# Performance work log

Hardware: AMD Instinct MI355X
Metric: run time of the kernel (lower is better)

The kernel has to match this reference:

```python
import jax, jax.numpy as jnp
import numpy as np

H = 1024
F = 3584
E = 8
TOP_K = 2
B, S = 2, 1024


def setup_inputs() -> dict:
    key = jax.random.key(0)
    ks = jax.random.split(key, 5)
    scale_h = 1.0 / np.sqrt(H)
    scale_f = 1.0 / np.sqrt(F)
    return {
        "hidden_states": jax.random.normal(ks[0], (B, S, H), dtype=jnp.float32),
        "gate_w": jax.random.normal(ks[1], (H, E), dtype=jnp.float32) * scale_h,
        "w1": jax.random.normal(ks[2], (E, H, F), dtype=jnp.float32) * scale_h,
        "w3": jax.random.normal(ks[3], (E, H, F), dtype=jnp.float32) * scale_h,
        "w2": jax.random.normal(ks[4], (E, F, H), dtype=jnp.float32) * scale_f,
        "top_k": TOP_K,
    }


def reference(hidden_states, gate_w, w1, w3, w2, top_k):
    b, s, h = hidden_states.shape
    e = gate_w.shape[1]
    x = hidden_states.reshape(-1, h)  # [N, H]

    # Router: softmax over experts, top-k selection, renormalize (Mixtral).
    logits = x @ gate_w                             # [N, E]
    probs = jax.nn.softmax(logits, axis=-1)
    rw, sel = jax.lax.top_k(probs, top_k)           # [N, K]
    rw = rw / jnp.sum(rw, axis=-1, keepdims=True)

    # Dispatch/combine weights: combine[n, e] = sum_k rw[n,k] * (sel[n,k]==e).
    # This is the mathematical equivalent of moe_permute + weighted moe_unpermute.
    combine = jnp.sum(jax.nn.one_hot(sel, e, dtype=rw.dtype) * rw[..., None], axis=1)  # [N, E]

    # Grouped SwiGLU expert MLPs; loop over the small fixed expert count so the
    # [N, F] intermediate is materialized one expert at a time.
    out = jnp.zeros_like(x)
    for ei in range(e):
        hdn = jax.nn.silu(x @ w1[ei]) * (x @ w3[ei])  # [N, F]
        out = out + combine[:, ei:ei + 1] * (hdn @ w2[ei])
    return out.reshape(b, s, h)
```

## Files before the change

kernel.cpp:

```cpp
#include <hip/hip_runtime.h>
#include <hip/hip_bf16.h>

#define NTOK 2048
#define HD   1024
#define FD   3584
#define NE   8

#define BM 128
#define BN1 64
#define BM2 64
#define BN 128
#define BK 64
#define NIT1 (HD / BK)
#define KS2 2
#define KLEN2 (FD / KS2)
#define NIT2 (KLEN2 / BK)

typedef __attribute__((ext_vector_type(8))) short short8;
typedef __attribute__((ext_vector_type(4))) float f32x4;

__device__ __forceinline__ unsigned short f2bf(float f) {
    __hip_bfloat16 h = __float2bfloat16(f);
    union { __hip_bfloat16 h; unsigned short u; } c; c.h = h;
    return c.u;
}

typedef __attribute__((address_space(1))) const unsigned int g_cu32;
typedef __attribute__((address_space(3))) unsigned int l_u32;
__device__ __forceinline__ void gl16(const void* g, void* l) {
    __builtin_amdgcn_global_load_lds((g_cu32*)g, (l_u32*)(unsigned int)(size_t)l, 16, 0, 0);
}

__global__ void k_router(const float* __restrict__ x, const float* __restrict__ gw,
                         int* __restrict__ sel, float* __restrict__ selw,
                         int* __restrict__ counts) {
    int token = blockIdx.x * 4 + (threadIdx.x >> 6);
    int lane  = threadIdx.x & 63;
    if (token >= NTOK) return;
    const float* xr = x + (size_t)token * HD;
    float acc[NE];
#pragma unroll
    for (int e = 0; e < NE; e++) acc[e] = 0.f;
    for (int h = lane; h < HD; h += 64) {
        float xv = xr[h];
        const float4* g = (const float4*)(gw + (size_t)h * NE);
        float4 g0 = g[0], g1 = g[1];
        acc[0] += xv * g0.x; acc[1] += xv * g0.y; acc[2] += xv * g0.z; acc[3] += xv * g0.w;
        acc[4] += xv * g1.x; acc[5] += xv * g1.y; acc[6] += xv * g1.z; acc[7] += xv * g1.w;
    }
#pragma unroll
    for (int e = 0; e < NE; e++) {
#pragma unroll
        for (int off = 32; off >= 1; off >>= 1) acc[e] += __shfl_xor(acc[e], off, 64);
    }
    if (lane == 0) {
        float m = acc[0];
#pragma unroll
        for (int e = 1; e < NE; e++) m = fmaxf(m, acc[e]);
        float z[NE];
#pragma unroll
        for (int e = 0; e < NE; e++) z[e] = expf(acc[e] - m);
        int e0 = 0; float z0 = z[0];
#pragma unroll
        for (int e = 1; e < NE; e++) if (z[e] > z0) { z0 = z[e]; e0 = e; }
        int e1 = -1; float z1 = -1.f;
#pragma unroll
        for (int e = 0; e < NE; e++) if (e != e0 && z[e] > z1) { z1 = z[e]; e1 = e; }
        float s = z0 + z1;
        sel[token * 2 + 0] = e0; sel[token * 2 + 1] = e1;
        selw[token * 2 + 0] = z0 / s; selw[token * 2 + 1] = z1 / s;
        atomicAdd(&counts[e0], 1);
        atomicAdd(&counts[e1], 1);
    }
}

__global__ void k_scan(const int* __restrict__ counts, int* __restrict__ basep,
                       int* __restrict__ fillc) {
    if (threadIdx.x == 0 && blockIdx.x == 0) {
        int b = 0;
        for (int e = 0; e < NE; e++) { basep[e] = b; b += counts[e]; fillc[e] = 0; }
    }
}

__global__ void k_fill(const int* __restrict__ sel, const float* __restrict__ selw,
                       const int* __restrict__ basep, int* __restrict__ fillc,
                       int* __restrict__ rowmap, int* __restrict__ rowk,
                       float* __restrict__ roww) {
    int n = blockIdx.x * blockDim.x + threadIdx.x;
    if (n >= NTOK) return;
#pragma unroll
    for (int k = 0; k < 2; k++) {
        int e = sel[n * 2 + k];
        int p = atomicAdd(&fillc[e], 1);
        int g = basep[e] + p;
        rowmap[g] = n; rowk[g] = k; roww[g] = selw[n * 2 + k];
    }
}

__global__ void k_cvt(const float* __restrict__ x, unsigned short* __restrict__ xb) {
    size_t i = ((size_t)blockIdx.x * blockDim.x + threadIdx.x) * 8;
    float4 a = *(const float4*)(x + i);
    float4 b = *(const float4*)(x + i + 4);
    unsigned short p[8] __attribute__((aligned(16))) =
        { f2bf(a.x), f2bf(a.y), f2bf(a.z), f2bf(a.w),
          f2bf(b.x), f2bf(b.y), f2bf(b.z), f2bf(b.w) };
    *(uint4*)(xb + i) = *(uint4*)p;
}

__device__ __forceinline__ uint4 pack8(const float4* bv, int c) {
#define BF(r) ((unsigned int)f2bf(((const float*)&bv[r])[c]))
    uint4 u;
    u.x = BF(0) | (BF(1) << 16);
    u.y = BF(2) | (BF(3) << 16);
    u.z = BF(4) | (BF(5) << 16);
    u.w = BF(6) | (BF(7) << 16);
#undef BF
    return u;
}

__global__ __launch_bounds__(256, 2) void k_gemm1(
    const unsigned short* __restrict__ xb,
    const float* __restrict__ w1, const float* __restrict__ w3,
    const int* __restrict__ counts, const int* __restrict__ basep,
    const int* __restrict__ rowmap, unsigned short* __restrict__ act)
{
    const int e = blockIdx.z;
    const int nrows = counts[e];
    const int m0 = blockIdx.y * BM;
    if (m0 >= nrows) return;
    const int f0 = blockIdx.x * BN1;
    const int gbase = basep[e];

    __shared__ __align__(16) unsigned short At[2][BM][BK];
    __shared__ __align__(16) unsigned short B1[2][BN1][BK];
    __shared__ __align__(16) unsigned short B3[2][BN1][BK];

    const int t = threadIdx.x;
    const int lane = t & 63;
    const int w = t >> 6;
    const int wrm = w >> 1, wnn = w & 1;
    const int lr = lane >> 3;
    const int so = ((lane & 7) ^ lr) * 8;

    const unsigned short* asrc[4];
#pragma unroll
    for (int c = 0; c < 4; c++) {
        const int row = (w * 4 + c) * 8 + lr;
        const int tok = rowmap[gbase + min(m0 + row, nrows - 1)];
        asrc[c] = xb + (size_t)tok * HD + so;
    }

    const int nq = t & 15;
    const int kt = (t >> 4) & 7;
    const int half = t >> 7;
    const float* bp = (half ? w3 : w1) + (size_t)e * HD * FD + (size_t)(8 * kt) * FD + f0 + 4 * nq;
    unsigned short* const bb = half ? &B3[0][0][0] : &B1[0][0][0];
    const int BUFS = BN1 * BK;

    f32x4 acc1[4][2], acc3[4][2];
#pragma unroll
    for (int i = 0; i < 4; i++)
#pragma unroll
        for (int j = 0; j < 2; j++) { acc1[i][j] = (f32x4)(0.f); acc3[i][j] = (f32x4)(0.f); }

    const int l15 = lane & 15;
    const int lhi = lane >> 4;
    const int rs = (l15 & 7) * 8;

    float4 bv[8];

#define G1_WRITE(buf_) do {                                                     \
    _Pragma("unroll")                                                           \
    for (int c = 0; c < 4; c++) {                                               \
        const int n = 4 * nq + c;                                               \
        *(uint4*)&bb[(buf_) * BUFS + n * BK + 8 * (kt ^ (n & 7))] = pack8(bv, c); \
    }                                                                           \
} while (0)

#pragma unroll
    for (int r = 0; r < 8; r++) bv[r] = *(const float4*)(bp + (size_t)r * FD);
#pragma unroll
    for (int c = 0; c < 4; c++) gl16(asrc[c], &At[0][(w * 4 + c) * 8][0]);
    G1_WRITE(0);
    if (NIT1 > 1) {
#pragma unroll
        for (int r = 0; r < 8; r++) bv[r] = *(const float4*)(bp + (size_t)(BK + r) * FD);
        asm volatile("s_waitcnt lgkmcnt(0)" ::: "memory");
        asm volatile("s_waitcnt vmcnt(8)" ::: "memory");
    } else {
        asm volatile("s_waitcnt lgkmcnt(0)" ::: "memory");
        asm volatile("s_waitcnt vmcnt(0)" ::: "memory");
    }
    __builtin_amdgcn_s_barrier();

    for (int it = 0; it < NIT1; ++it) {
        const int cur = it & 1;
        const bool more = (it + 1 < NIT1);
        const bool more2 = (it + 2 < NIT1);
        if (more) {
#pragma unroll
            for (int c = 0; c < 4; c++)
                gl16(asrc[c] + (size_t)(it + 1) * BK, &At[cur ^ 1][(w * 4 + c) * 8][0]);
            G1_WRITE(cur ^ 1);
            if (more2) {
                const size_t k0 = (size_t)(it + 2) * BK;
#pragma unroll
                for (int r = 0; r < 8; r++) bv[r] = *(const float4*)(bp + (k0 + r) * FD);
            }
        }
#pragma unroll
        for (int kk = 0; kk < 2; kk++) {
            const int kc = (kk * 32 + lhi * 8) ^ rs;
            short8 af[4], b1f[2], b3f[2];
#pragma unroll
            for (int i = 0; i < 4; i++)
                af[i] = *(const short8*)&At[cur][wrm * 64 + i * 16 + l15][kc];
#pragma unroll
            for (int j = 0; j < 2; j++) {
                b1f[j] = *(const short8*)&B1[cur][wnn * 32 + j * 16 + l15][kc];
                b3f[j] = *(const short8*)&B3[cur][wnn * 32 + j * 16 + l15][kc];
            }
#pragma unroll
            for (int i = 0; i < 4; i++)
#pragma unroll
                for (int j = 0; j < 2; j++) {
                    acc1[i][j] = __builtin_amdgcn_mfma_f32_16x16x32_bf16(af[i], b1f[j], acc1[i][j], 0, 0, 0);
                    acc3[i][j] = __builtin_amdgcn_mfma_f32_16x16x32_bf16(af[i], b3f[j], acc3[i][j], 0, 0, 0);
                }
        }
        if (more) {
            asm volatile("s_waitcnt lgkmcnt(0)" ::: "memory");
            if (more2) asm volatile("s_waitcnt vmcnt(8)" ::: "memory");
            else       asm volatile("s_waitcnt vmcnt(0)" ::: "memory");
        }
        __builtin_amdgcn_s_barrier();
    }

    const int rbase = wrm * 64 + lhi * 4;
    const int cbase = f0 + wnn * 32 + l15;
#pragma unroll
    for (int i = 0; i < 4; i++) {
#pragma unroll
        for (int r = 0; r < 4; r++) {
            const int ml = rbase + i * 16 + r;
            if (m0 + ml < nrows) {
                const size_t rowoff = (size_t)(gbase + m0 + ml) * FD;
#pragma unroll
                for (int j = 0; j < 2; j++) {
                    float y1 = acc1[i][j][r];
                    float y3 = acc3[i][j][r];
                    float sv = (y1 / (1.f + __expf(-y1))) * y3;
                    act[rowoff + cbase + j * 16] = f2bf(sv);
                }
            }
        }
    }
#undef G1_WRITE
}

__global__ __launch_bounds__(256, 3) void k_gemm2(
    const unsigned short* __restrict__ act,
    const float* __restrict__ w2,
    const int* __restrict__ counts, const int* __restrict__ basep,
    const int* __restrict__ rowmap, const int* __restrict__ rowk,
    const float* __restrict__ roww, float* __restrict__ partial)
{
    const int z = blockIdx.z;
    const int e = z >> 1, ks = z & 1;
    const int nrows = counts[e];
    const int m0 = blockIdx.y * BM2;
    if (m0 >= nrows) return;
    const int h0 = blockIdx.x * BN;
    const int gbase = basep[e];
    const int kbase = ks * KLEN2;

    __shared__ __align__(16) unsigned short At[2][BM2][BK];
    __shared__ __align__(16) unsigned short Bt[2][BN][BK];

    const int t = threadIdx.x;
    const int lane = t & 63;
    const int w = t >> 6;
    const int wr2 = w >> 1, wn2 = w & 1;
    const int lr = lane >> 3;
    const int so = ((lane & 7) ^ lr) * 8;

    const unsigned short* asrc[2];
#pragma unroll
    for (int c = 0; c < 2; c++) {
        const int row = (w * 2 + c) * 8 + lr;
        asrc[c] = act + ((size_t)gbase + min(m0 + row, nrows - 1)) * FD + so + kbase;
    }

    const int nq = (lane & 15) | ((w >> 1) << 4);
    const int kt = ((lane >> 4) & 3) | ((w & 1) << 2);
    const float* bp = w2 + (size_t)e * FD * HD + (size_t)(kbase + 8 * kt) * HD + h0 + 4 * nq;
    unsigned short* const bb = &Bt[0][0][0];
    const int BUFS2 = BN * BK;

    f32x4 acc[2][4];
#pragma unroll
    for (int i = 0; i < 2; i++)
#pragma unroll
        for (int j = 0; j < 4; j++) acc[i][j] = (f32x4)(0.f);

    const int l15 = lane & 15;
    const int lhi = lane >> 4;
    const int rs = (l15 & 7) * 8;

    float4 bv[8];

#define G2_WRITE(buf_) do {                                                     \
    _Pragma("unroll")                                                           \
    for (int c = 0; c < 4; c++) {                                               \
        const int n = 4 * nq + c;                                               \
        *(uint4*)&bb[(buf_) * BUFS2 + n * BK + 8 * (kt ^ (n & 7))] = pack8(bv, c); \
    }                                                                           \
} while (0)

#pragma unroll
    for (int r = 0; r < 8; r++) bv[r] = *(const float4*)(bp + (size_t)r * HD);
#pragma unroll
    for (int c = 0; c < 2; c++) gl16(asrc[c], &At[0][(w * 2 + c) * 8][0]);
    G2_WRITE(0);
    if (NIT2 > 1) {
#pragma unroll
        for (int r = 0; r < 8; r++) bv[r] = *(const float4*)(bp + (size_t)(BK + r) * HD);
        asm volatile("s_waitcnt lgkmcnt(0)" ::: "memory");
        asm volatile("s_waitcnt vmcnt(8)" ::: "memory");
    } else {
        asm volatile("s_waitcnt lgkmcnt(0)" ::: "memory");
        asm volatile("s_waitcnt vmcnt(0)" ::: "memory");
    }
    __builtin_amdgcn_s_barrier();

    for (int it = 0; it < NIT2; ++it) {
        const int cur = it & 1;
        const bool more = (it + 1 < NIT2);
        const bool more2 = (it + 2 < NIT2);
        if (more) {
#pragma unroll
            for (int c = 0; c < 2; c++)
                gl16(asrc[c] + (size_t)(it + 1) * BK, &At[cur ^ 1][(w * 2 + c) * 8][0]);
            G2_WRITE(cur ^ 1);
            if (more2) {
                const size_t k0 = (size_t)(it + 2) * BK;
#pragma unroll
                for (int r = 0; r < 8; r++) bv[r] = *(const float4*)(bp + (k0 + r) * HD);
            }
        }
#pragma unroll
        for (int kk = 0; kk < 2; kk++) {
            const int kc = (kk * 32 + lhi * 8) ^ rs;
            short8 af[2], bf[4];
#pragma unroll
            for (int i = 0; i < 2; i++)
                af[i] = *(const short8*)&At[cur][wr2 * 32 + i * 16 + l15][kc];
#pragma unroll
            for (int j = 0; j < 4; j++)
                bf[j] = *(const short8*)&Bt[cur][wn2 * 64 + j * 16 + l15][kc];
#pragma unroll
            for (int i = 0; i < 2; i++)
#pragma unroll
                for (int j = 0; j < 4; j++)
                    acc[i][j] = __builtin_amdgcn_mfma_f32_16x16x32_bf16(af[i], bf[j], acc[i][j], 0, 0, 0);
        }
        if (more) {
            asm volatile("s_waitcnt lgkmcnt(0)" ::: "memory");
            if (more2) asm volatile("s_waitcnt vmcnt(8)" ::: "memory");
            else       asm volatile("s_waitcnt vmcnt(0)" ::: "memory");
        }
        __builtin_amdgcn_s_barrier();
    }

    const int rbase = wr2 * 32 + lhi * 4;
    const int cbase = h0 + wn2 * 64 + l15;
#pragma unroll
    for (int i = 0; i < 2; i++) {
#pragma unroll
        for (int r = 0; r < 4; r++) {
            const int ml = rbase + i * 16 + r;
            if (m0 + ml < nrows) {
                const int grow = gbase + m0 + ml;
                const int tok = rowmap[grow];
                const int slot = rowk[grow];
                const float wv = roww[grow];
                float* op = partial + (((size_t)slot * KS2 + ks) * NTOK + tok) * HD + cbase;
#pragma unroll
                for (int j = 0; j < 4; j++) op[j * 16] = acc[i][j][r] * wv;
            }
        }
    }
#undef G2_WRITE
}

__global__ void k_combine(const float* __restrict__ partial, float* __restrict__ out) {
    size_t i = ((size_t)blockIdx.x * blockDim.x + threadIdx.x) * 4;
    const size_t st = (size_t)NTOK * HD;
    float4 o = *(const float4*)(partial + i);
#pragma unroll
    for (int s = 1; s < 2 * KS2; s++) {
        float4 v = *(const float4*)(partial + (size_t)s * st + i);
        o.x += v.x; o.y += v.y; o.z += v.z; o.w += v.w;
    }
    *(float4*)(out + i) = o;
}

extern "C" void kernel_launch(void* const* d_in, const int* in_sizes, int n_in,
                              void* d_out, int out_size, void* d_ws, size_t ws_size,
                              hipStream_t stream) {
    const float* x  = (const float*)d_in[0];
    const float* gw = (const float*)d_in[1];
    const float* w1 = (const float*)d_in[2];
    const float* w3 = (const float*)d_in[3];
    const float* w2 = (const float*)d_in[4];
    float* out = (float*)d_out;

    char* ws = (char*)d_ws;
    size_t off = 0;
    auto alloc = [&](size_t b) { char* p = ws + off; off += (b + 255) & ~(size_t)255; return p; };
    int*   sel    = (int*)  alloc((size_t)NTOK * 2 * 4);
    float* selw   = (float*)alloc((size_t)NTOK * 2 * 4);
    int*   counts = (int*)  alloc(NE * 4);
    int*   basep  = (int*)  alloc(NE * 4);
    int*   fillc  = (int*)  alloc(NE * 4);
    int*   rowmap = (int*)  alloc((size_t)NTOK * 2 * 4);
    int*   rowk   = (int*)  alloc((size_t)NTOK * 2 * 4);
    float* roww   = (float*)alloc((size_t)NTOK * 2 * 4);
    unsigned short* xb  = (unsigned short*)alloc((size_t)NTOK * HD * 2);
    unsigned short* act = (unsigned short*)alloc((size_t)NTOK * 2 * FD * 2);
    float* partial = (float*)alloc((size_t)2 * KS2 * NTOK * HD * 4);

    hipMemsetAsync(counts, 0, NE * 4, stream);
    k_cvt<<<(NTOK * HD) / (256 * 8), 256, 0, stream>>>(x, xb);
    k_router<<<NTOK / 4, 256, 0, stream>>>(x, gw, sel, selw, counts);
    k_scan<<<1, 64, 0, stream>>>(counts, basep, fillc);
    k_fill<<<NTOK / 256, 256, 0, stream>>>(sel, selw, basep, fillc, rowmap, rowk, roww);
    k_gemm1<<<dim3(FD / BN1, NTOK / BM, NE), 256, 0, stream>>>(xb, w1, w3, counts, basep, rowmap, act);
    k_gemm2<<<dim3(HD / BN, NTOK / BM2, NE * KS2), 256, 0, stream>>>(act, w2, counts, basep, rowmap, rowk, roww, partial);
    k_combine<<<(NTOK * HD) / (256 * 4), 256, 0, stream>>>(partial, out);
}
```

Before: 342.0 us.

## Repack weight tiles as paired-k bf16 words and atomically accumulate expert outputs

Both expert GEMMs now stage the fp32 weight tile into shared memory as 32-bit words, each holding two consecutive k values for one output column. The tile uses a new XOR swizzle, and each thread loads two k-rows of 16 columns, aiming for cheaper conversion, better coalescing and fewer bank conflicts. The second GEMM also drops the partial buffer and the combine kernel, adding its weighted results into a zeroed output with float atomics. This removes a large partial-buffer write and read plus one launch, at the cost of atomic contention and non-deterministic summation order.

Measured after the change: 355.3 us. 3.9% more time.

```diff
diff --git a/kernel.cpp b/kernel.cpp
--- a/kernel.cpp
+++ b/kernel.cpp
@@ -31,6 +31,12 @@
     __builtin_amdgcn_global_load_lds((g_cu32*)g, (l_u32*)(unsigned int)(size_t)l, 16, 0, 0);
 }
 
+__device__ __forceinline__ short8 pfrag(const unsigned int* P, int n, int q) {
+    uint4 v = *(const uint4*)&P[n * 32 + 4 * ((q ^ (n >> 3)) & 7)];
+    union { uint4 u; short8 s; } c; c.u = v;
+    return c.s;
+}
+
 __global__ void k_router(const float* __restrict__ x, const float* __restrict__ gw,
                          int* __restrict__ sel, float* __restrict__ selw,
                          int* __restrict__ counts) {
@@ -105,17 +111,6 @@
         { f2bf(a.x), f2bf(a.y), f2bf(a.z), f2bf(a.w),
           f2bf(b.x), f2bf(b.y), f2bf(b.z), f2bf(b.w) };
     *(uint4*)(xb + i) = *(uint4*)p;
-}
-
-__device__ __forceinline__ uint4 pack8(const float4* bv, int c) {
-#define BF(r) ((unsigned int)f2bf(((const float*)&bv[r])[c]))
-    uint4 u;
-    u.x = BF(0) | (BF(1) << 16);
-    u.y = BF(2) | (BF(3) << 16);
-    u.z = BF(4) | (BF(5) << 16);
-    u.w = BF(6) | (BF(7) << 16);
-#undef BF
-    return u;
 }
 
 __global__ __launch_bounds__(256, 2) void k_gemm1(
@@ -132,8 +127,8 @@
     const int gbase = basep[e];
 
     __shared__ __align__(16) unsigned short At[2][BM][BK];
-    __shared__ __align__(16) unsigned short B1[2][BN1][BK];
-    __shared__ __align__(16) unsigned short B3[2][BN1][BK];
+    __shared__ __align__(16) unsigned int P1[2][BN1 * 32];
+    __shared__ __align__(16) unsigned int P3[2][BN1 * 32];
 
     const int t = threadIdx.x;
     const int lane = t & 63;
@@ -150,12 +145,14 @@
         asrc[c] = xb + (size_t)tok * HD + so;
     }
 
-    const int nq = t & 15;
-    const int kt = (t >> 4) & 7;
+    const int th = t & 127;
+    const int rp = th >> 2;
+    const int c4 = th & 3;
     const int half = t >> 7;
-    const float* bp = (half ? w3 : w1) + (size_t)e * HD * FD + (size_t)(8 * kt) * FD + f0 + 4 * nq;
-    unsigned short* const bb = half ? &B3[0][0][0] : &B1[0][0][0];
-    const int BUFS = BN1 * BK;
+    const float* bp = (half ? w3 : w1) + (size_t)e * HD * FD
+                    + (size_t)(2 * rp) * FD + f0 + c4 * 16;
+    unsigned int* const myP = half ? &P3[0][0] : &P1[0][0];
+    const int PB = BN1 * 32;
 
     f32x4 acc1[4][2], acc3[4][2];
 #pragma unroll
@@ -167,30 +164,36 @@
     const int lhi = lane >> 4;
     const int rs = (l15 & 7) * 8;
 
-    float4 bv[8];
-
-#define G1_WRITE(buf_) do {                                                     \
+    float4 bv0[4], bv1[4];
+
+#define G1_LOADB(koff_) do {                                                    \
     _Pragma("unroll")                                                           \
-    for (int c = 0; c < 4; c++) {                                               \
-        const int n = 4 * nq + c;                                               \
-        *(uint4*)&bb[(buf_) * BUFS + n * BK + 8 * (kt ^ (n & 7))] = pack8(bv, c); \
+    for (int m = 0; m < 4; m++) {                                               \
+        bv0[m] = *(const float4*)(bp + (size_t)(koff_) * FD + 4 * m);           \
+        bv1[m] = *(const float4*)(bp + (size_t)((koff_) + 1) * FD + 4 * m);     \
     }                                                                           \
 } while (0)
 
-#pragma unroll
-    for (int r = 0; r < 8; r++) bv[r] = *(const float4*)(bp + (size_t)r * FD);
+#define G1_WRITEB(buf_) do {                                                    \
+    _Pragma("unroll")                                                           \
+    for (int m = 0; m < 4; m++) {                                               \
+        _Pragma("unroll")                                                       \
+        for (int q = 0; q < 4; q++) {                                           \
+            const int n = c4 * 16 + 4 * m + q;                                  \
+            unsigned int v = (unsigned int)f2bf(((const float*)&bv0[m])[q])     \
+                           | ((unsigned int)f2bf(((const float*)&bv1[m])[q]) << 16); \
+            myP[(buf_) * PB + n * 32 + (rp ^ (((n >> 3) & 7) << 2))] = v;       \
+        }                                                                       \
+    }                                                                           \
+} while (0)
+
+    G1_LOADB(0);
+    G1_WRITEB(0);
 #pragma unroll
     for (int c = 0; c < 4; c++) gl16(asrc[c], &At[0][(w * 4 + c) * 8][0]);
-    G1_WRITE(0);
-    if (NIT1 > 1) {
-#pragma unroll
-        for (int r = 0; r < 8; r++) bv[r] = *(const float4*)(bp + (size_t)(BK + r) * FD);
-        asm volatile("s_waitcnt lgkmcnt(0)" ::: "memory");
-        asm volatile("s_waitcnt vmcnt(8)" ::: "memory");
-    } else {
-        asm volatile("s_waitcnt lgkmcnt(0)" ::: "memory");
-        asm volatile("s_waitcnt vmcnt(0)" ::: "memory");
-    }
+    if (NIT1 > 1) G1_LOADB(BK);
+    asm volatile("s_waitcnt lgkmcnt(0)" ::: "memory");
+    asm volatile("s_waitcnt vmcnt(8)" ::: "memory");
     __builtin_amdgcn_s_barrier();
 
     for (int it = 0; it < NIT1; ++it) {
@@ -201,24 +204,22 @@
 #pragma unroll
             for (int c = 0; c < 4; c++)
                 gl16(asrc[c] + (size_t)(it + 1) * BK, &At[cur ^ 1][(w * 4 + c) * 8][0]);
-            G1_WRITE(cur ^ 1);
-            if (more2) {
-                const size_t k0 = (size_t)(it + 2) * BK;
-#pragma unroll
-                for (int r = 0; r < 8; r++) bv[r] = *(const float4*)(bp + (k0 + r) * FD);
-            }
+            G1_WRITEB(cur ^ 1);
+            if (more2) G1_LOADB((size_t)(it + 2) * BK);
         }
 #pragma unroll
         for (int kk = 0; kk < 2; kk++) {
             const int kc = (kk * 32 + lhi * 8) ^ rs;
+            const int q = kk * 4 + lhi;
             short8 af[4], b1f[2], b3f[2];
 #pragma unroll
             for (int i = 0; i < 4; i++)
                 af[i] = *(const short8*)&At[cur][wrm * 64 + i * 16 + l15][kc];
 #pragma unroll
             for (int j = 0; j < 2; j++) {
-                b1f[j] = *(const short8*)&B1[cur][wnn * 32 + j * 16 + l15][kc];
-                b3f[j] = *(const short8*)&B3[cur][wnn * 32 + j * 16 + l15][kc];
+                const int n = wnn * 32 + j * 16 + l15;
+                b1f[j] = pfrag(&P1[cur][0], n, q);
+                b3f[j] = pfrag(&P3[cur][0], n, q);
             }
 #pragma unroll
             for (int i = 0; i < 4; i++)
@@ -255,7 +256,8 @@
             }
         }
     }
-#undef G1_WRITE
+#undef G1_LOADB
+#undef G1_WRITEB
 }
 
 __global__ __launch_bounds__(256, 3) void k_gemm2(
@@ -263,7 +265,7 @@
     const float* __restrict__ w2,
     const int* __restrict__ counts, const int* __restrict__ basep,
     const int* __restrict__ rowmap, const int* __restrict__ rowk,
-    const float* __restrict__ roww, float* __restrict__ partial)
+    const float* __restrict__ roww, float* __restrict__ out)
 {
     const int z = blockIdx.z;
     const int e = z >> 1, ks = z & 1;
@@ -275,7 +277,7 @@
     const int kbase = ks * KLEN2;
 
     __shared__ __align__(16) unsigned short At[2][BM2][BK];
-    __shared__ __align__(16) unsigned short Bt[2][BN][BK];
+    __shared__ __align__(16) unsigned int P[2][BN * 32];
 
     const int t = threadIdx.x;
     const int lane = t & 63;
@@ -291,11 +293,9 @@
         asrc[c] = act + ((size_t)gbase + min(m0 + row, nrows - 1)) * FD + so + kbase;
     }
 
-    const int nq = (lane & 15) | ((w >> 1) << 4);
-    const int kt = ((lane >> 4) & 3) | ((w & 1) << 2);
-    const float* bp = w2 + (size_t)e * FD * HD + (size_t)(kbase + 8 * kt) * HD + h0 + 4 * nq;
-    unsigned short* const bb = &Bt[0][0][0];
-    const int BUFS2 = BN * BK;
+    const int rp = t >> 3;
+    const int c8 = t & 7;
+    const float* bp = w2 + (size_t)e * FD * HD + (size_t)(kbase + 2 * rp) * HD + h0 + c8 * 16;
 
     f32x4 acc[2][4];
 #pragma unroll
@@ -307,30 +307,36 @@
     const int lhi = lane >> 4;
     const int rs = (l15 & 7) * 8;
 
-    float4 bv[8];
-
-#define G2_WRITE(buf_) do {                                                     \
+    float4 bv0[4], bv1[4];
+
+#define G2_LOADB(koff_) do {                                                    \
     _Pragma("unroll")                                                           \
-    for (int c = 0; c < 4; c++) {                                               \
-        const int n = 4 * nq + c;                                               \
-        *(uint4*)&bb[(buf_) * BUFS2 + n * BK + 8 * (kt ^ (n & 7))] = pack8(bv, c); \
+    for (int m = 0; m < 4; m++) {                                               \
+        bv0[m] = *(const float4*)(bp + (size_t)(koff_) * HD + 4 * m);           \
+        bv1[m] = *(const float4*)(bp + (size_t)((koff_) + 1) * HD + 4 * m);     \
     }                                                                           \
 } while (0)
 
-#pragma unroll
-    for (int r = 0; r < 8; r++) bv[r] = *(const float4*)(bp + (size_t)r * HD);
+#define G2_WRITEB(buf_) do {                                                    \
+    _Pragma("unroll")                                                           \
+    for (int m = 0; m < 4; m++) {                                               \
+        _Pragma("unroll")                                                       \
+        for (int q = 0; q < 4; q++) {                                           \
+            const int n = c8 * 16 + 4 * m + q;                                  \
+            unsigned int v = (unsigned int)f2bf(((const float*)&bv0[m])[q])     \
+                           | ((unsigned int)f2bf(((const float*)&bv1[m])[q]) << 16); \
+            P[buf_][n * 32 + (rp ^ (((n >> 3) & 7) << 2))] = v;                 \
+        }                                                                       \
+    }                                                                           \
+} while (0)
+
+    G2_LOADB(0);
+    G2_WRITEB(0);
 #pragma unroll
     for (int c = 0; c < 2; c++) gl16(asrc[c], &At[0][(w * 2 + c) * 8][0]);
-    G2_WRITE(0);
-    if (NIT2 > 1) {
-#pragma unroll
-        for (int r = 0; r < 8; r++) bv[r] = *(const float4*)(bp + (size_t)(BK + r) * HD);
-        asm volatile("s_waitcnt lgkmcnt(0)" ::: "memory");
-        asm volatile("s_waitcnt vmcnt(8)" ::: "memory");
-    } else {
-        asm volatile("s_waitcnt lgkmcnt(0)" ::: "memory");
-        asm volatile("s_waitcnt vmcnt(0)" ::: "memory");
-    }
+    if (NIT2 > 1) G2_LOADB(BK);
+    asm volatile("s_waitcnt lgkmcnt(0)" ::: "memory");
+    asm volatile("s_waitcnt vmcnt(8)" ::: "memory");
     __builtin_amdgcn_s_barrier();
 
     for (int it = 0; it < NIT2; ++it) {
@@ -341,23 +347,22 @@
 #pragma unroll
             for (int c = 0; c < 2; c++)
                 gl16(asrc[c] + (size_t)(it + 1) * BK, &At[cur ^ 1][(w * 2 + c) * 8][0]);
-            G2_WRITE(cur ^ 1);
-            if (more2) {
-                const size_t k0 = (size_t)(it + 2) * BK;
-#pragma unroll
-                for (int r = 0; r < 8; r++) bv[r] = *(const float4*)(bp + (k0 + r) * HD);
-            }
+            G2_WRITEB(cur ^ 1);
+            if (more2) G2_LOADB((size_t)(it + 2) * BK);
         }
 #pragma unroll
         for (int kk = 0; kk < 2; kk++) {
             const int kc = (kk * 32 + lhi * 8) ^ rs;
+            const int q = kk * 4 + lhi;
             short8 af[2], bf[4];
 #pragma unroll
             for (int i = 0; i < 2; i++)
                 af[i] = *(const short8*)&At[cur][wr2 * 32 + i * 16 + l15][kc];
 #pragma unroll
-            for (int j = 0; j < 4; j++)
-                bf[j] = *(const short8*)&Bt[cur][wn2 * 64 + j * 16 + l15][kc];
+            for (int j = 0; j < 4; j++) {
+                const int n = wn2 * 64 + j * 16 + l15;
+                bf[j] = pfrag(&P[cur][0], n, q);
+            }
 #pragma unroll
             for (int i = 0; i < 2; i++)
 #pragma unroll
@@ -382,27 +387,16 @@
             if (m0 + ml < nrows) {
                 const int grow = gbase + m0 + ml;
                 const int tok = rowmap[grow];
-                const int slot = rowk[grow];
                 const float wv = roww[grow];
-                float* op = partial + (((size_t)slot * KS2 + ks) * NTOK + tok) * HD + cbase;
-#pragma unroll
-                for (int j = 0; j < 4; j++) op[j * 16] = acc[i][j][r] * wv;
+                float* op = out + (size_t)tok * HD + cbase;
+#pragma unroll
+                for (int j = 0; j < 4; j++)
+                    atomicAdd(&op[j * 16], acc[i][j][r] * wv);
             }
         }
     }
-#undef G2_WRITE
-}
-
-__global__ void k_combine(const float* __restrict__ partial, float* __restrict__ out) {
-    size_t i = ((size_t)blockIdx.x * blockDim.x + threadIdx.x) * 4;
-    const size_t st = (size_t)NTOK * HD;
-    float4 o = *(const float4*)(partial + i);
-#pragma unroll
-    for (int s = 1; s < 2 * KS2; s++) {
-        float4 v = *(const float4*)(partial + (size_t)s * st + i);
-        o.x += v.x; o.y += v.y; o.z += v.z; o.w += v.w;
-    }
-    *(float4*)(out + i) = o;
+#undef G2_LOADB
+#undef G2_WRITEB
 }
 
 extern "C" void kernel_launch(void* const* d_in, const int* in_sizes, int n_in,
@@ -428,14 +422,13 @@
     float* roww   = (float*)alloc((size_t)NTOK * 2 * 4);
     unsigned short* xb  = (unsigned short*)alloc((size_t)NTOK * HD * 2);
     unsigned short* act = (unsigned short*)alloc((size_t)NTOK * 2 * FD * 2);
-    float* partial = (float*)alloc((size_t)2 * KS2 * NTOK * HD * 4);
 
     hipMemsetAsync(counts, 0, NE * 4, stream);
+    hipMemsetAsync(out, 0, (size_t)out_size * 4, stream);
     k_cvt<<<(NTOK * HD) / (256 * 8), 256, 0, stream>>>(x, xb);
     k_router<<<NTOK / 4, 256, 0, stream>>>(x, gw, sel, selw, counts);
     k_scan<<<1, 64, 0, stream>>>(counts, basep, fillc);
     k_fill<<<NTOK / 256, 256, 0, stream>>>(sel, selw, basep, fillc, rowmap, rowk, roww);
     k_gemm1<<<dim3(FD / BN1, NTOK / BM, NE), 256, 0, stream>>>(xb, w1, w3, counts, basep, rowmap, act);
-    k_gemm2<<<dim3(HD / BN, NTOK / BM2, NE * KS2), 256, 0, stream>>>(act, w2, counts, basep, rowmap, rowk, roww, partial);
-    k_combine<<<(NTOK * HD) / (256 * 4), 256, 0, stream>>>(partial, out);
-}
+    k_gemm2<<<dim3(HD / BN, NTOK / BM2, NE * KS2), 256, 0, stream>>>(act, w2, counts, basep, rowmap, rowk, roww, out);
+}
```
